# Kernel tuning notes

Measured on AMD Instinct MI355X. Metric: run time of the kernel, lower is better.

Reference implementation:

```python
import jax, jax.numpy as jnp
import numpy as np

SPS_AMPLIFY = 1.5
SPS_DAMPEN = 0.3
SPS_DEEP_QUESTION = 0.1
SPS_EXCLAIM = 0.85
SPS_QUESTION = 0.25
SPS_SUPER_EXCLAIM = 0.95

B, S, D = 4, 2048, 1024
NUM_HEADS = 16
HEAD_DIM = D // NUM_HEADS
SCALE = HEAD_DIM ** (-0.5)


def sps_pro(x):
    """Piecewise elementwise modulation based on sigmoid(x) bands."""
    xn = jax.nn.sigmoid(x)
    # bands: xn>0.95 -> 2.0 ; 0.85<xn<=0.95 -> 1.5 ; xn<0.1 -> 0.1 ;
    #        0.1<=xn<0.25 -> 0.3 ; else -> 1.0
    mult = jnp.where(
        xn > SPS_SUPER_EXCLAIM, 2.0,
        jnp.where(xn > SPS_EXCLAIM, SPS_AMPLIFY,
                  jnp.where(xn < SPS_DEEP_QUESTION, 0.1,
                            jnp.where(xn < SPS_QUESTION, SPS_DAMPEN, 1.0))))
    return x * mult


def setup_inputs() -> dict:
    key = jax.random.key(0)
    k0, k1, k2, k3, k4 = jax.random.split(key, 5)
    s = 1.0 / np.sqrt(D)
    return {
        "x": jax.random.normal(k0, (B, S, D), dtype=jnp.float32),
        "W_qkv": jax.random.uniform(k1, (D, 3 * D), dtype=jnp.float32, minval=-s, maxval=s),
        "b_qkv": jax.random.uniform(k2, (3 * D,), dtype=jnp.float32, minval=-s, maxval=s),
        "W_proj": jax.random.uniform(k3, (D, D), dtype=jnp.float32, minval=-s, maxval=s),
        "b_proj": jax.random.uniform(k4, (D,), dtype=jnp.float32, minval=-s, maxval=s),
    }


def reference(x, W_qkv, b_qkv, W_proj, b_proj):
    qkv = jnp.einsum('bsd,de->bse', x, W_qkv) + b_qkv  # [B,S,3D]
    q, k, v = jnp.split(qkv, 3, axis=-1)               # each [B,S,D]
    attn = jnp.einsum('bsd,btd->bst', q, k) * SCALE    # [B,S,S]
    attn = sps_pro(attn)
    attn = jax.nn.softmax(attn, axis=-1)
    out = jnp.einsum('bst,btd->bsd', attn, v)          # [B,S,D]
    out = jnp.einsum('bsd,de->bse', out, W_proj) + b_proj
    return out
```

## Files before the change

### kernel.cpp

```cpp
#include <hip/hip_runtime.h>
#include <hip/hip_bf16.h>
#include <hip/hip_fp16.h>
#include <stdint.h>

typedef __attribute__((ext_vector_type(8))) _Float16 f16x8;
typedef __attribute__((ext_vector_type(4))) float f32x4;

__device__ __forceinline__ void async16(void* lds, const void* g) {
  __builtin_amdgcn_global_load_lds(
      (const __attribute__((address_space(1))) void*)g,
      (__attribute__((address_space(3))) void*)lds, 16, 0, 0);
}

__device__ __forceinline__ uint16_t f2h_u(float f) {
  union { __half h; uint16_t u; } c;
  c.h = __float2half(f);
  return c.u;
}

__global__ __launch_bounds__(256)
void prep_all(const float* __restrict__ x, uint16_t* __restrict__ xh,
              const float* __restrict__ Wqkv, uint16_t* __restrict__ WqkvT,
              const float* __restrict__ Wproj, uint16_t* __restrict__ WpT) {
  const int bid = blockIdx.x;
  if (bid < 2048) {
    const int base = bid * 256 + threadIdx.x;
#pragma unroll
    for (int k = 0; k < 4; ++k) {
      const int i = base + k * 524288;
      float4 v = ((const float4*)x)[i];
      ushort4 o;
      o.x = f2h_u(v.x); o.y = f2h_u(v.y); o.z = f2h_u(v.z); o.w = f2h_u(v.w);
      ((ushort4*)xh)[i] = o;
    }
  } else {
    __shared__ float t[64][65];
    const float* in;
    uint16_t* out;
    int ldin, ldout, r0, c0;
    if (bid < 2816) {
      const int id = bid - 2048;
      in = Wqkv; out = WqkvT; ldin = 3072; ldout = 1024;
      c0 = (id % 48) * 64; r0 = (id / 48) * 64;
    } else {
      const int id = bid - 2816;
      in = Wproj; out = WpT; ldin = 1024; ldout = 1024;
      c0 = (id % 16) * 64; r0 = (id / 16) * 64;
    }
    const int tx = threadIdx.x & 63, ty = threadIdx.x >> 6;
#pragma unroll
    for (int i = 0; i < 16; ++i)
      t[ty + i * 4][tx] = in[(size_t)(r0 + ty + i * 4) * ldin + c0 + tx];
    __syncthreads();
#pragma unroll
    for (int i = 0; i < 16; ++i)
      out[(size_t)(c0 + ty + i * 4) * ldout + r0 + tx] = f2h_u(t[tx][ty + i * 4]);
  }
}

template <int EPI>
__global__ __launch_bounds__(512, 2)
void gemm8p(const uint16_t* __restrict__ A, const uint16_t* __restrict__ B,
            void* __restrict__ Cv, void* __restrict__ Cv2,
            const float* __restrict__ bias,
            int nT, int lda, int ldb, int ldc,
            long long strA, long long strB, long long strC) {
  extern __shared__ uint16_t lds_u16[];

  const int gx = gridDim.x, gy = gridDim.y;
  const int nwg = gx * gy * gridDim.z;
  const int fid = blockIdx.x + gx * (blockIdx.y + gy * blockIdx.z);
  const int fs = (fid & 7) * (nwg >> 3) + (fid >> 3);
  const int bx = fs % gx;
  const int by = (fs / gx) % gy;
  const int bz = fs / (gx * gy);

  const int tid = threadIdx.x;
  const int l = tid & 63;
  const int w = tid >> 6;
  const int wm = w >> 2, wn = w & 3;
  const int l15 = l & 15, l4 = l >> 4;
  const int rowBase = bx * 256, colBase = by * 256;
  const uint16_t* Ag = A + (size_t)bz * strA;
  const uint16_t* Bg = B + (size_t)bz * strB;

  const uint16_t* sA[2][2];
  const uint16_t* sB[2][2];
#pragma unroll
  for (int u = 0; u < 2; ++u) {
    int c = tid + (u << 9);
    int cs = c ^ ((c >> 3) & 7);
    int row = cs >> 3, kc = (cs & 7) * 8;
    sA[0][u] = Ag + (size_t)(rowBase + row) * lda + kc;
    sA[1][u] = Ag + (size_t)(rowBase + 128 + row) * lda + kc;
    sB[0][u] = Bg + (size_t)(colBase + row) * ldb + kc;
    sB[1][u] = Bg + (size_t)(colBase + 128 + row) * ldb + kc;
  }

  f32x4 acc[8][4];
#pragma unroll
  for (int m = 0; m < 8; ++m)
#pragma unroll
    for (int n = 0; n < 4; ++n)
      acc[m][n] = (f32x4){0.f, 0.f, 0.f, 0.f};

#define SH_A(buf, h, koff)                                                     \
  {                                                                            \
    const uint32_t d_ = (buf)*32768u + (h)*8192u;                              \
    async16(&lds_u16[d_ + (size_t)tid * 8], sA[h][0] + (koff));                \
    async16(&lds_u16[d_ + (size_t)(tid + 512) * 8], sA[h][1] + (koff));        \
  }
#define SH_B(buf, h, koff)                                                     \
  {                                                                            \
    const uint32_t d_ = (buf)*32768u + 16384u + (h)*8192u;                     \
    async16(&lds_u16[d_ + (size_t)tid * 8], sB[h][0] + (koff));                \
    async16(&lds_u16[d_ + (size_t)(tid + 512) * 8], sB[h][1] + (koff));        \
  }
#define RD_A(dst, buf, mh)                                                     \
  _Pragma("unroll") for (int mr = 0; mr < 4; ++mr) {                           \
    const int lr = (mh)*64 + mr * 16 + l15;                                    \
    const char* hb = (const char*)lds_u16 + (buf)*65536 + wm * 16384;          \
    _Pragma("unroll") for (int ks = 0; ks < 2; ++ks)                           \
      dst[mr][ks] = *(const f16x8*)(hb + lr * 128 +                            \
                    ((ks * 64 + l4 * 16) ^ ((lr & 7) << 4)));                  \
  }
#define RD_B(dst, buf, nh)                                                     \
  _Pragma("unroll") for (int nr = 0; nr < 2; ++nr) {                           \
    const int lr = (wn & 1) * 64 + (nh)*32 + nr * 16 + l15;                    \
    const char* hb = (const char*)lds_u16 + (buf)*65536 + 32768 +              \
                     (wn >> 1) * 16384;                                        \
    _Pragma("unroll") for (int ks = 0; ks < 2; ++ks)                           \
      dst[nr][ks] = *(const f16x8*)(hb + lr * 128 +                            \
                    ((ks * 64 + l4 * 16) ^ ((lr & 7) << 4)));                  \
  }
#define MM(m0, n0, AF, BF)                                                     \
  __builtin_amdgcn_s_setprio(1);                                               \
  _Pragma("unroll") for (int ks = 0; ks < 2; ++ks)                             \
  _Pragma("unroll") for (int mr = 0; mr < 4; ++mr)                             \
  _Pragma("unroll") for (int nr = 0; nr < 2; ++nr)                             \
    acc[(m0) + mr][(n0) + nr] = __builtin_amdgcn_mfma_f32_16x16x32_f16(        \
        AF[mr][ks], BF[nr][ks], acc[(m0) + mr][(n0) + nr], 0, 0, 0);           \
  __builtin_amdgcn_s_setprio(0);
#define VMC(n) asm volatile("s_waitcnt vmcnt(" #n ")" ::: "memory");
#define BAR() __builtin_amdgcn_s_barrier();

  SH_A(0, 0, 0) SH_A(0, 1, 0) SH_B(0, 0, 0) SH_B(0, 1, 0)
  SH_B(1, 0, 64) SH_B(1, 1, 64)
  VMC(4)
  BAR()

  const int nIter = nT >> 1;
  for (int i = 0; i < nIter; ++i) {
    const int e2 = 2 * i + 2, o = 2 * i + 1, o2 = 2 * i + 3;
    const int ke2 = e2 << 6, ko = o << 6, ko2 = o2 << 6;
    f16x8 a0[4][2], a1[4][2], b0[2][2], b1[2][2];
    RD_A(a0, 0, 0) RD_B(b0, 0, 0)
    SH_A(1, 0, ko)
    BAR()
    MM(0, 0, a0, b0)
    RD_B(b1, 0, 1)
    SH_A(1, 1, ko)
    BAR()
    MM(0, 2, a0, b1)
    RD_A(a1, 0, 1)
    if (e2 < nT) SH_B(0, 0, ke2)
    BAR()
    MM(4, 2, a1, b1)
    if (e2 < nT) { SH_B(0, 1, ke2) VMC(4) } else { VMC(0) }
    BAR()
    MM(4, 0, a1, b0)
    RD_A(a0, 1, 0) RD_B(b0, 1, 0)
    if (e2 < nT) SH_A(0, 0, ke2)
    BAR()
    MM(0, 0, a0, b0)
    RD_B(b1, 1, 1)
    if (e2 < nT) SH_A(0, 1, ke2)
    BAR()
    MM(0, 2, a0, b1)
    RD_A(a1, 1, 1)
    if (o2 < nT) SH_B(1, 0, ko2)
    BAR()
    MM(4, 2, a1, b1)
    if (o2 < nT) { SH_B(1, 1, ko2) }
    if (i + 1 < nIter) { if (o2 < nT) { VMC(4) } else { VMC(0) } }
    BAR()
    MM(4, 0, a1, b0)
  }
#undef SH_A
#undef SH_B
#undef RD_A
#undef RD_B
#undef MM
#undef VMC
#undef BAR

  if (EPI == 0) {
    uint16_t* qd = (uint16_t*)Cv;
    uint16_t* kd = (uint16_t*)Cv2;
#pragma unroll
    for (int ni = 0; ni < 4; ++ni) {
      const int gcol = colBase + wn * 64 + ni * 16 + l15;
      const float bv = bias[gcol];
      uint16_t* base = (gcol < 1024 ? qd : kd) + (gcol & 1023);
#pragma unroll
      for (int mi = 0; mi < 8; ++mi)
#pragma unroll
        for (int j = 0; j < 4; ++j) {
          const int grow = rowBase + wm * 128 + mi * 16 + l4 * 4 + j;
          base[(size_t)(grow >> 11) * 2097152 + (size_t)(grow & 2047) * 1024] =
              f2h_u(acc[mi][ni][j] + bv);
        }
    }
  }
}

template <int EPI>
__global__ __launch_bounds__(256, 2)
void gemm_mb(const uint16_t* __restrict__ A, const uint16_t* __restrict__ B,
             void* __restrict__ Cv, const float* __restrict__ bias,
             float* __restrict__ rowsum,
             int nT, int lda, int ldb, int ldc,
             long long strA, long long strB, long long strC) {
  extern __shared__ uint16_t lds_u16[];

  const int gx = gridDim.x, gy = gridDim.y;
  const int nwg = gx * gy * gridDim.z;
  const int fid = blockIdx.x + gx * (blockIdx.y + gy * blockIdx.z);
  const int fs = (fid & 7) * (nwg >> 3) + (fid >> 3);
  const int bx = fs % gx;
  const int by = (fs / gx) % gy;
  const int bz = fs / (gx * gy);

  const int tid = threadIdx.x;
  const int l = tid & 63;
  const int w = tid >> 6;
  const int wm = w >> 1, wn = w & 1;
  const int l15 = l & 15, l4 = l >> 4;
  const int rowBase = bx * 128, colBase = by * 128;
  const uint16_t* Ag = A + (size_t)bz * strA;
  const uint16_t* Bg = B + (size_t)bz * strB;

  const uint16_t* pA[4];
  const uint16_t* pB[4];
#pragma unroll
  for (int u = 0; u < 4; ++u) {
    int c = tid + (u << 8);
    int cs = c ^ ((c >> 3) & 7);
    pA[u] = Ag + (size_t)(rowBase + (cs >> 3)) * lda + (cs & 7) * 8;
    pB[u] = Bg + (size_t)(colBase + (cs >> 3)) * ldb + (cs & 7) * 8;
  }

  f32x4 acc[4][4];
#pragma unroll
  for (int m = 0; m < 4; ++m)
#pragma unroll
    for (int n = 0; n < 4; ++n)
      acc[m][n] = (f32x4){0.f, 0.f, 0.f, 0.f};

#define STAGE(t2, s2)                                                          \
  {                                                                            \
    const int kb_ = (t2) << 6;                                                 \
    uint16_t* dA_ = lds_u16 + (s2)*16384;                                      \
    uint16_t* dB_ = dA_ + 8192;                                                \
    _Pragma("unroll") for (int u = 0; u < 4; ++u) {                            \
      async16(&dA_[(size_t)(tid + (u << 8)) * 8], pA[u] + kb_);                \
      async16(&dB_[(size_t)(tid + (u << 8)) * 8], pB[u] + kb_);                \
    }                                                                          \
  }

  STAGE(0, 0)
  asm volatile("s_waitcnt vmcnt(0)" ::: "memory");
  __builtin_amdgcn_s_barrier();

  for (int t = 0; t < nT; ++t) {
    const int s = t & 1;
    if (t + 1 < nT) STAGE(t + 1, s ^ 1)
    const uint16_t* As = lds_u16 + s * 16384;
    const uint16_t* Bs = As + 8192;
#pragma unroll
    for (int ks = 0; ks < 2; ++ks) {
      f16x8 af[4], bf[4];
#pragma unroll
      for (int m = 0; m < 4; ++m) {
        const int r = wm * 64 + m * 16 + l15;
        const int byt = r * 128 + ((ks * 64 + l4 * 16) ^ ((r & 7) << 4));
        af[m] = *(const f16x8*)((const char*)As + byt);
      }
#pragma unroll
      for (int n = 0; n < 4; ++n) {
        const int r = wn * 64 + n * 16 + l15;
        const int byt = r * 128 + ((ks * 64 + l4 * 16) ^ ((r & 7) << 4));
        bf[n] = *(const f16x8*)((const char*)Bs + byt);
      }
      __builtin_amdgcn_s_setprio(1);
#pragma unroll
      for (int m = 0; m < 4; ++m)
#pragma unroll
        for (int n = 0; n < 4; ++n)
          acc[m][n] = __builtin_amdgcn_mfma_f32_16x16x32_f16(af[m], bf[n], acc[m][n], 0, 0, 0);
      __builtin_amdgcn_s_setprio(0);
    }
    if (t + 1 < nT) {
      asm volatile("s_waitcnt vmcnt(0)" ::: "memory");
      __builtin_amdgcn_s_barrier();
    }
  }
#undef STAGE

  const int orow0 = rowBase + wm * 64 + l4 * 4;
  const int ocol0 = colBase + wn * 64 + l15;
  if (EPI == 2) {
    uint16_t* C = (uint16_t*)Cv + (size_t)bz * strC;
#pragma unroll
    for (int m = 0; m < 4; ++m)
#pragma unroll
      for (int j = 0; j < 4; ++j) {
        const int d = orow0 + m * 16 + j;
        const float bv = bias[d];
#pragma unroll
        for (int n = 0; n < 4; ++n)
          C[(size_t)d * ldc + ocol0 + n * 16] = f2h_u(acc[m][n][j] + bv);
      }
  } else if (EPI == 5) {
    uint16_t* C = (uint16_t*)Cv + (size_t)bz * strC;
    float* rs_b = rowsum + (size_t)bz * 2048;
#pragma unroll
    for (int m = 0; m < 4; ++m)
#pragma unroll
      for (int j = 0; j < 4; ++j) {
        const int grow = orow0 + m * 16 + j;
        float rs = 0.f;
#pragma unroll
        for (int n = 0; n < 4; ++n) {
          float xs = acc[m][n][j] * 0.125f;
          float mult = (xs > 2.94443897916644f) ? 2.0f
                     : (xs > 1.73460105538811f) ? 1.5f
                     : (xs < -2.19722457733622f) ? 0.1f
                     : (xs < -1.09861228866811f) ? 0.3f
                                                 : 1.0f;
          float e = __expf(fminf(xs * mult, 19.0f) - 8.0f);
          C[(size_t)grow * ldc + ocol0 + n * 16] = f2h_u(e);
          rs += e;
        }
        rs += __shfl_xor(rs, 1);
        rs += __shfl_xor(rs, 2);
        rs += __shfl_xor(rs, 4);
        rs += __shfl_xor(rs, 8);
        if (l15 == 0) atomicAdd(&rs_b[grow], rs);
      }
  } else if (EPI == 6) {
    uint16_t* C = (uint16_t*)Cv + (size_t)bz * strC;
    const float* rs_b = rowsum + (size_t)bz * 2048;
#pragma unroll
    for (int m = 0; m < 4; ++m)
#pragma unroll
      for (int j = 0; j < 4; ++j) {
        const int grow = orow0 + m * 16 + j;
        const float inv = 1.0f / rs_b[grow];
#pragma unroll
        for (int n = 0; n < 4; ++n)
          C[(size_t)grow * ldc + ocol0 + n * 16] = f2h_u(acc[m][n][j] * inv);
      }
  } else {
    float* C = (float*)Cv;
#pragma unroll
    for (int n = 0; n < 4; ++n) {
      const float bv = bias[ocol0 + n * 16];
#pragma unroll
      for (int m = 0; m < 4; ++m)
#pragma unroll
        for (int j = 0; j < 4; ++j)
          C[(size_t)(orow0 + m * 16 + j) * ldc + ocol0 + n * 16] = acc[m][n][j] + bv;
    }
  }
}

extern "C" void kernel_launch(void* const* d_in, const int* in_sizes, int n_in,
                              void* d_out, int out_size, void* d_ws, size_t ws_size,
                              hipStream_t stream) {
  const float* x     = (const float*)d_in[0];
  const float* Wqkv  = (const float*)d_in[1];
  const float* bqkv  = (const float*)d_in[2];
  const float* Wproj = (const float*)d_in[3];
  const float* bproj = (const float*)d_in[4];
  float* out = (float*)d_out;

  char* ws = (char*)d_ws;
  size_t off = 0;
  auto alloc = [&](size_t bytes) -> void* {
    void* p = ws + off;
    off += (bytes + 255) & ~(size_t)255;
    return p;
  };
  uint16_t* xh     = (uint16_t*)alloc(8192ULL * 1024 * 2);
  uint16_t* WqkvT  = (uint16_t*)alloc(3072ULL * 1024 * 2);
  uint16_t* WpT    = (uint16_t*)alloc(1024ULL * 1024 * 2);
  uint16_t* qh     = (uint16_t*)alloc(4ULL * 2048 * 1024 * 2);
  uint16_t* kh     = (uint16_t*)alloc(4ULL * 2048 * 1024 * 2);
  uint16_t* vT     = (uint16_t*)alloc(4ULL * 1024 * 2048 * 2);
  uint16_t* Pm     = (uint16_t*)alloc(4ULL * 2048 * 2048 * 2);
  float*    rowsum = (float*)alloc(4ULL * 2048 * 4);
  uint16_t* ao     = xh;

  hipMemsetAsync(rowsum, 0, 4ULL * 2048 * 4, stream);
  prep_all<<<3072, 256, 0, stream>>>(x, xh, Wqkv, WqkvT, Wproj, WpT);
  gemm8p<0><<<dim3(32, 8, 1), 512, 131072, stream>>>(
      xh, WqkvT, qh, kh, bqkv, 16, 1024, 1024, 0, 0, 0, 0);
  gemm_mb<2><<<dim3(8, 16, 4), 256, 65536, stream>>>(
      WqkvT + 2048ULL * 1024, xh, vT, bqkv + 2048, nullptr,
      16, 1024, 1024, 2048, 0, 2097152LL, 2097152LL);
  gemm_mb<5><<<dim3(16, 16, 4), 256, 65536, stream>>>(
      qh, kh, Pm, nullptr, rowsum, 16, 1024, 1024, 2048,
      2097152LL, 2097152LL, 4194304LL);
  gemm_mb<6><<<dim3(16, 8, 4), 256, 65536, stream>>>(
      Pm, vT, ao, nullptr, rowsum, 32, 2048, 2048, 1024,
      4194304LL, 2097152LL, 2097152LL);
  gemm_mb<4><<<dim3(64, 8, 1), 256, 65536, stream>>>(
      ao, WpT, out, bproj, nullptr, 16, 1024, 1024, 1024, 0, 0, 0);
}
```

Before: 203.8 us.

## Use 256x128 tile with triple-buffered LDS pipeline for QK^T score GEMM

Adds a new gemm_r3 kernel for the QK^T + sps/exp epilogue. It uses 512 threads (8 waves) on a 256x128 output tile and a 3-stage LDS ring with partial vmcnt waits, so the load for tile t+2 is in flight while tile t is computed. The goal is better reuse of the K tile and better hiding of global-load latency. In exchange it needs 144 KB of LDS per block, which at most allows one block per CU, and the grid is halved in the row dimension.

```diff
diff --git a/kernel.cpp b/kernel.cpp
--- a/kernel.cpp
+++ b/kernel.cpp
@@ -215,10 +215,9 @@
 }
 
 template <int EPI>
-__global__ __launch_bounds__(256, 2)
-void gemm_mb(const uint16_t* __restrict__ A, const uint16_t* __restrict__ B,
-             void* __restrict__ Cv, const float* __restrict__ bias,
-             float* __restrict__ rowsum,
+__global__ __launch_bounds__(512, 2)
+void gemm_r3(const uint16_t* __restrict__ A, const uint16_t* __restrict__ B,
+             void* __restrict__ Cv, float* __restrict__ rowsum,
              int nT, int lda, int ldb, int ldc,
              long long strA, long long strB, long long strC) {
   extern __shared__ uint16_t lds_u16[];
@@ -236,17 +235,22 @@
   const int w = tid >> 6;
   const int wm = w >> 1, wn = w & 1;
   const int l15 = l & 15, l4 = l >> 4;
-  const int rowBase = bx * 128, colBase = by * 128;
+  const int rowBase = bx * 256, colBase = by * 128;
   const uint16_t* Ag = A + (size_t)bz * strA;
   const uint16_t* Bg = B + (size_t)bz * strB;
 
   const uint16_t* pA[4];
-  const uint16_t* pB[4];
+  const uint16_t* pB[2];
 #pragma unroll
   for (int u = 0; u < 4; ++u) {
-    int c = tid + (u << 8);
+    int c = tid + (u << 9);
     int cs = c ^ ((c >> 3) & 7);
     pA[u] = Ag + (size_t)(rowBase + (cs >> 3)) * lda + (cs & 7) * 8;
+  }
+#pragma unroll
+  for (int u = 0; u < 2; ++u) {
+    int c = tid + (u << 9);
+    int cs = c ^ ((c >> 3) & 7);
     pB[u] = Bg + (size_t)(colBase + (cs >> 3)) * ldb + (cs & 7) * 8;
   }
 
@@ -260,23 +264,25 @@
 #define STAGE(t2, s2)                                                          \
   {                                                                            \
     const int kb_ = (t2) << 6;                                                 \
-    uint16_t* dA_ = lds_u16 + (s2)*16384;                                      \
-    uint16_t* dB_ = dA_ + 8192;                                                \
-    _Pragma("unroll") for (int u = 0; u < 4; ++u) {                            \
-      async16(&dA_[(size_t)(tid + (u << 8)) * 8], pA[u] + kb_);                \
-      async16(&dB_[(size_t)(tid + (u << 8)) * 8], pB[u] + kb_);                \
-    }                                                                          \
+    uint16_t* dA_ = lds_u16 + (s2) * 24576;                                    \
+    uint16_t* dB_ = dA_ + 16384;                                               \
+    _Pragma("unroll") for (int u = 0; u < 4; ++u)                              \
+        async16(&dA_[(size_t)(tid + (u << 9)) * 8], pA[u] + kb_);              \
+    _Pragma("unroll") for (int u = 0; u < 2; ++u)                              \
+        async16(&dB_[(size_t)(tid + (u << 9)) * 8], pB[u] + kb_);              \
   }
 
   STAGE(0, 0)
-  asm volatile("s_waitcnt vmcnt(0)" ::: "memory");
+  STAGE(1, 1)
+  asm volatile("s_waitcnt vmcnt(6)" ::: "memory");
   __builtin_amdgcn_s_barrier();
 
+  int sl = 0;
   for (int t = 0; t < nT; ++t) {
-    const int s = t & 1;
-    if (t + 1 < nT) STAGE(t + 1, s ^ 1)
-    const uint16_t* As = lds_u16 + s * 16384;
-    const uint16_t* Bs = As + 8192;
+    int s2 = sl + 2; if (s2 >= 3) s2 -= 3;
+    if (t + 2 < nT) STAGE(t + 2, s2)
+    const uint16_t* As = lds_u16 + sl * 24576;
+    const uint16_t* Bs = As + 16384;
 #pragma unroll
     for (int ks = 0; ks < 2; ++ks) {
       f16x8 af[4], bf[4];
@@ -301,27 +307,20 @@
       __builtin_amdgcn_s_setprio(0);
     }
     if (t + 1 < nT) {
-      asm volatile("s_waitcnt vmcnt(0)" ::: "memory");
+      if (t + 2 < nT) {
+        asm volatile("s_waitcnt vmcnt(6)" ::: "memory");
+      } else {
+        asm volatile("s_waitcnt vmcnt(0)" ::: "memory");
+      }
       __builtin_amdgcn_s_barrier();
     }
+    sl = (sl == 2) ? 0 : sl + 1;
   }
 #undef STAGE
 
   const int orow0 = rowBase + wm * 64 + l4 * 4;
   const int ocol0 = colBase + wn * 64 + l15;
-  if (EPI == 2) {
-    uint16_t* C = (uint16_t*)Cv + (size_t)bz * strC;
-#pragma unroll
-    for (int m = 0; m < 4; ++m)
-#pragma unroll
-      for (int j = 0; j < 4; ++j) {
-        const int d = orow0 + m * 16 + j;
-        const float bv = bias[d];
-#pragma unroll
-        for (int n = 0; n < 4; ++n)
-          C[(size_t)d * ldc + ocol0 + n * 16] = f2h_u(acc[m][n][j] + bv);
-      }
-  } else if (EPI == 5) {
+  if (EPI == 5) {
     uint16_t* C = (uint16_t*)Cv + (size_t)bz * strC;
     float* rs_b = rowsum + (size_t)bz * 2048;
 #pragma unroll
@@ -348,6 +347,116 @@
         rs += __shfl_xor(rs, 8);
         if (l15 == 0) atomicAdd(&rs_b[grow], rs);
       }
+  }
+}
+
+template <int EPI>
+__global__ __launch_bounds__(256, 2)
+void gemm_mb(const uint16_t* __restrict__ A, const uint16_t* __restrict__ B,
+             void* __restrict__ Cv, const float* __restrict__ bias,
+             float* __restrict__ rowsum,
+             int nT, int lda, int ldb, int ldc,
+             long long strA, long long strB, long long strC) {
+  extern __shared__ uint16_t lds_u16[];
+
+  const int gx = gridDim.x, gy = gridDim.y;
+  const int nwg = gx * gy * gridDim.z;
+  const int fid = blockIdx.x + gx * (blockIdx.y + gy * blockIdx.z);
+  const int fs = (fid & 7) * (nwg >> 3) + (fid >> 3);
+  const int bx = fs % gx;
+  const int by = (fs / gx) % gy;
+  const int bz = fs / (gx * gy);
+
+  const int tid = threadIdx.x;
+  const int l = tid & 63;
+  const int w = tid >> 6;
+  const int wm = w >> 1, wn = w & 1;
+  const int l15 = l & 15, l4 = l >> 4;
+  const int rowBase = bx * 128, colBase = by * 128;
+  const uint16_t* Ag = A + (size_t)bz * strA;
+  const uint16_t* Bg = B + (size_t)bz * strB;
+
+  const uint16_t* pA[4];
+  const uint16_t* pB[4];
+#pragma unroll
+  for (int u = 0; u < 4; ++u) {
+    int c = tid + (u << 8);
+    int cs = c ^ ((c >> 3) & 7);
+    pA[u] = Ag + (size_t)(rowBase + (cs >> 3)) * lda + (cs & 7) * 8;
+    pB[u] = Bg + (size_t)(colBase + (cs >> 3)) * ldb + (cs & 7) * 8;
+  }
+
+  f32x4 acc[4][4];
+#pragma unroll
+  for (int m = 0; m < 4; ++m)
+#pragma unroll
+    for (int n = 0; n < 4; ++n)
+      acc[m][n] = (f32x4){0.f, 0.f, 0.f, 0.f};
+
+#define STAGE(t2, s2)                                                          \
+  {                                                                            \
+    const int kb_ = (t2) << 6;                                                 \
+    uint16_t* dA_ = lds_u16 + (s2)*16384;                                      \
+    uint16_t* dB_ = dA_ + 8192;                                                \
+    _Pragma("unroll") for (int u = 0; u < 4; ++u) {                            \
+      async16(&dA_[(size_t)(tid + (u << 8)) * 8], pA[u] + kb_);                \
+      async16(&dB_[(size_t)(tid + (u << 8)) * 8], pB[u] + kb_);                \
+    }                                                                          \
+  }
+
+  STAGE(0, 0)
+  asm volatile("s_waitcnt vmcnt(0)" ::: "memory");
+  __builtin_amdgcn_s_barrier();
+
+  for (int t = 0; t < nT; ++t) {
+    const int s = t & 1;
+    if (t + 1 < nT) STAGE(t + 1, s ^ 1)
+    const uint16_t* As = lds_u16 + s * 16384;
+    const uint16_t* Bs = As + 8192;
+#pragma unroll
+    for (int ks = 0; ks < 2; ++ks) {
+      f16x8 af[4], bf[4];
+#pragma unroll
+      for (int m = 0; m < 4; ++m) {
+        const int r = wm * 64 + m * 16 + l15;
+        const int byt = r * 128 + ((ks * 64 + l4 * 16) ^ ((r & 7) << 4));
+        af[m] = *(const f16x8*)((const char*)As + byt);
+      }
+#pragma unroll
+      for (int n = 0; n < 4; ++n) {
+        const int r = wn * 64 + n * 16 + l15;
+        const int byt = r * 128 + ((ks * 64 + l4 * 16) ^ ((r & 7) << 4));
+        bf[n] = *(const f16x8*)((const char*)Bs + byt);
+      }
+      __builtin_amdgcn_s_setprio(1);
+#pragma unroll
+      for (int m = 0; m < 4; ++m)
+#pragma unroll
+        for (int n = 0; n < 4; ++n)
+          acc[m][n] = __builtin_amdgcn_mfma_f32_16x16x32_f16(af[m], bf[n], acc[m][n], 0, 0, 0);
+      __builtin_amdgcn_s_setprio(0);
+    }
+    if (t + 1 < nT) {
+      asm volatile("s_waitcnt vmcnt(0)" ::: "memory");
+      __builtin_amdgcn_s_barrier();
+    }
+  }
+#undef STAGE
+
+  const int orow0 = rowBase + wm * 64 + l4 * 4;
+  const int ocol0 = colBase + wn * 64 + l15;
+  if (EPI == 2) {
+    uint16_t* C = (uint16_t*)Cv + (size_t)bz * strC;
+#pragma unroll
+    for (int m = 0; m < 4; ++m)
+#pragma unroll
+      for (int j = 0; j < 4; ++j) {
+        const int d = orow0 + m * 16 + j;
+        const float bv = bias[d];
+#pragma unroll
+        for (int n = 0; n < 4; ++n)
+          C[(size_t)d * ldc + ocol0 + n * 16] = f2h_u(acc[m][n][j] + bv);
+      }
   } else if (EPI == 6) {
     uint16_t* C = (uint16_t*)Cv + (size_t)bz * strC;
     const float* rs_b = rowsum + (size_t)bz * 2048;
@@ -409,8 +518,8 @@
   gemm_mb<2><<<dim3(8, 16, 4), 256, 65536, stream>>>(
       WqkvT + 2048ULL * 1024, xh, vT, bqkv + 2048, nullptr,
       16, 1024, 1024, 2048, 0, 2097152LL, 2097152LL);
-  gemm_mb<5><<<dim3(16, 16, 4), 256, 65536, stream>>>(
-      qh, kh, Pm, nullptr, rowsum, 16, 1024, 1024, 2048,
+  gemm_r3<5><<<dim3(8, 16, 4), 512, 147456, stream>>>(
+      qh, kh, Pm, rowsum, 16, 1024, 1024, 2048,
       2097152LL, 2097152LL, 4194304LL);
   gemm_mb<6><<<dim3(16, 8, 4), 256, 65536, stream>>>(
       Pm, vT, ao, nullptr, rowsum, 32, 2048, 2048, 1024,
```

New measurement: 204.9 us. No clear change (+0.6%).
